# Kernel tuning notes

Hardware: AMD Instinct MI355X
Metric: run time of the kernel (lower is better)

## Reference

```python
import jax, jax.numpy as jnp
import numpy as np
import math

B, S, D, H = 2, 2048, 1024, 16
HD = D // H  # head_dim = 64
ROPE_BASE = 100000
EPS = 1e-09


def _linear_init(key, in_f, out_f):
    std = min(1.0, math.sqrt(out_f / in_f)) / math.sqrt(in_f)
    return jax.random.normal(key, (in_f, out_f)) * std


def setup_inputs() -> dict:
    key = jax.random.key(0)
    ks = jax.random.split(key, 7)
    Q = jax.random.normal(ks[0], (B, S, D), dtype=jnp.float32)
    K = jax.random.normal(ks[1], (B, S, D), dtype=jnp.float32)
    V = jax.random.normal(ks[2], (B, S, D), dtype=jnp.float32)
    mask = jnp.tril(jnp.ones((S, S), dtype=bool))  # causal
    Wq = _linear_init(ks[3], D, D)
    Wk = _linear_init(ks[4], D, D)
    Wv = _linear_init(ks[5], D, D)
    Wo = _linear_init(ks[6], D, D)
    return {"Q": Q, "K": K, "V": V, "mask": mask,
            "Wq": Wq, "Wk": Wk, "Wv": Wv, "Wo": Wo}


def _rope_tables(seq_len, d):
    positions = jnp.arange(0, seq_len)
    freqs = ROPE_BASE ** (jnp.arange(0, d, 2) / d)
    gamma = positions[:, None] * (1.0 / freqs)[None, :]  # [t, d/2]
    return jnp.cos(gamma).astype(jnp.bfloat16), jnp.sin(gamma).astype(jnp.bfloat16)


def _apply_rope(x, cos, sin):
    # x: [..., t, d]; cos/sin: [t, d/2]
    d = x.shape[-1]
    x1, x2 = x[..., : d // 2], x[..., d // 2:]
    y1 = x1 * cos + x2 * sin
    y2 = -x1 * sin + x2 * cos
    return jnp.concatenate([y1, y2], axis=-1)


def _rms_norm(x):
    rms = jnp.sqrt(jnp.mean(jnp.square(x), axis=-1, keepdims=True) + EPS)
    return x / rms


def reference(Q, K, V, mask, Wq, Wk, Wv, Wo):
    cos, sin = _rope_tables(S, HD)
    q = jnp.dot(Q, Wq)
    k = jnp.dot(K, Wk)
    v = jnp.dot(V, Wv)
    # [B, S, D] -> [B, H, S, HD]
    split = lambda t: t.reshape(*t.shape[:-1], H, HD).swapaxes(-3, -2)
    q, k, v = split(q), split(k), split(v)
    q = _rms_norm(_apply_rope(q, cos, sin))
    k = _rms_norm(_apply_rope(k, cos, sin))
    logits = jnp.einsum('bhqd,bhkd->bhqk', q, k) / jnp.sqrt(jnp.float32(HD))
    logits = jnp.where(mask[None, None, :, :], logits, -1000000000.0)
    attn = jax.nn.softmax(logits, axis=-1)
    vals = jnp.einsum('bhqk,bhkd->bhqd', attn, v)
    # [B, H, S, HD] -> [B, S, D]
    vals = vals.swapaxes(-3, -2).reshape(B, S, D)
    return jnp.dot(vals, Wo)
```

## Files before the change

kernel.cpp:

```cpp
#include <hip/hip_runtime.h>
#include <hip/hip_bf16.h>
#include <stdint.h>

typedef __hip_bfloat16 bf16;
typedef __attribute__((ext_vector_type(8))) short short8;
typedef __attribute__((ext_vector_type(4))) float float4v;

static constexpr int nB = 2, nS = 2048, nD = 1024, nH = 16, nHD = 64;
static constexpr int nBS = nB * nS;

#define AS_GLOBAL __attribute__((address_space(1)))
#define AS_LDS    __attribute__((address_space(3)))

union Frag16B { short8 v; uint4 u4; uint2 u2[2]; };

__device__ __forceinline__ void gload_lds16(const void* g, void* l) {
  __builtin_amdgcn_global_load_lds((AS_GLOBAL uint32_t*)(g), (AS_LDS uint32_t*)(l), 16, 0, 0);
}

__device__ __forceinline__ float fast_exp2(float x) {
#if __has_builtin(__builtin_amdgcn_exp2f)
  return __builtin_amdgcn_exp2f(x);
#else
  float r; asm volatile("v_exp_f32 %0, %1" : "=v"(r) : "v"(x)); return r;
#endif
}

__device__ __forceinline__ void lds_barrier() {
  asm volatile("s_waitcnt lgkmcnt(0)\ns_barrier" ::: "memory");
}

__global__ __launch_bounds__(256) void prep_kernel(
    const float* __restrict__ Qin, const float* __restrict__ Kin, const float* __restrict__ Vin,
    const float* __restrict__ Wq, const float* __restrict__ Wk,
    const float* __restrict__ Wv, const float* __restrict__ Wo,
    bf16* __restrict__ Qbf, bf16* __restrict__ Kbf, bf16* __restrict__ Vbf,
    bf16* __restrict__ WqT, bf16* __restrict__ WkT, bf16* __restrict__ WvT, bf16* __restrict__ WoT,
    bf16* __restrict__ cos_t, bf16* __restrict__ sin_t) {
  __shared__ float tile[64][65];
  int bx = blockIdx.x, t = threadIdx.x;
  if (bx < 3072) {
    int tz = bx >> 10, blk = bx & 1023;
    const float* src = tz == 0 ? Qin : tz == 1 ? Kin : Vin;
    bf16* dst = tz == 0 ? Qbf : tz == 1 ? Kbf : Vbf;
#pragma unroll
    for (int i = 0; i < 4; ++i) {
      int idx = blk * 1024 + i * 256 + t;
      float4 v = ((const float4*)src)[idx];
      union { bf16 b[4]; uint2 u; } tmp;
      tmp.b[0] = __float2bfloat16(v.x);
      tmp.b[1] = __float2bfloat16(v.y);
      tmp.b[2] = __float2bfloat16(v.z);
      tmp.b[3] = __float2bfloat16(v.w);
      ((uint2*)dst)[idx] = tmp.u;
    }
  } else if (bx < 4096) {
    int idx = bx - 3072;
    int z = idx >> 8;
    const float* W = z == 0 ? Wq : z == 1 ? Wk : z == 2 ? Wv : Wo;
    bf16* T = z == 0 ? WqT : z == 1 ? WkT : z == 2 ? WvT : WoT;
    int tk = (idx & 15) * 64, tn = ((idx >> 4) & 15) * 64;
    int c = t & 63, r0 = t >> 6;
#pragma unroll
    for (int i = 0; i < 16; ++i) {
      int r = i * 4 + r0;
      tile[r][c] = W[(size_t)(tk + r) * nD + tn + c];
    }
    __syncthreads();
#pragma unroll
    for (int i = 0; i < 16; ++i) {
      int r = i * 4 + r0;
      T[(size_t)(tn + r) * nD + tk + c] = __float2bfloat16(tile[c][r]);
    }
  } else {
    int base = (bx - 4096) * 1024 + t * 4;
#pragma unroll
    for (int i = 0; i < 4; ++i) {
      int e = base + i;
      int s = e >> 5, j = e & 31;
      float inv_freq = powf(100000.0f, -(float)(2 * j) / 64.0f);
      float g = (float)s * inv_freq;
      cos_t[e] = __float2bfloat16(cosf(g));
      sin_t[e] = __float2bfloat16(sinf(g));
    }
  }
}

__global__ __launch_bounds__(256) void gemm_qkv_kernel(
    const bf16* __restrict__ A0, const bf16* __restrict__ A1, const bf16* __restrict__ A2,
    const bf16* __restrict__ Bt0, const bf16* __restrict__ Bt1, const bf16* __restrict__ Bt2,
    bf16* __restrict__ q_h, bf16* __restrict__ k_h, bf16* __restrict__ vt_h,
    const bf16* __restrict__ cos_t, const bf16* __restrict__ sin_t) {
  const int z = blockIdx.z;
  const bf16* A  = z == 0 ? A0 : (z == 1 ? A1 : A2);
  const bf16* Bt = z == 0 ? Bt0 : (z == 1 ? Bt1 : Bt2);

  __shared__ bf16 As[128 * 32];
  __shared__ bf16 Bs[128 * 32];

  const int t = threadIdx.x;
  const int lane = t & 63;
  const int wid = t >> 6;
  const int quad = lane >> 4;
  const int l16 = lane & 15;
  const int wm = wid >> 1;
  const int wn = wid & 1;
  const int m0 = blockIdx.y * 128;
  const int n0 = blockIdx.x * 128;
  const int K = nD;

  float4v acc[4][4] = {};

  for (int kt = 0; kt < K; kt += 32) {
    __syncthreads();
#pragma unroll
    for (int p = 0; p < 2; ++p) {
      int cch = p * 256 + wid * 64 + lane;
      int row = cch >> 2, cc = cch & 3;
      gload_lds16(A + (size_t)(m0 + row) * K + kt + cc * 8, As + (size_t)(p * 256 + wid * 64) * 8);
      gload_lds16(Bt + (size_t)(n0 + row) * K + kt + cc * 8, Bs + (size_t)(p * 256 + wid * 64) * 8);
    }
    __syncthreads();

    Frag16B a[4], b[4];
#pragma unroll
    for (int mi = 0; mi < 4; ++mi)
      a[mi].u4 = *(const uint4*)&As[(wm * 64 + mi * 16 + l16) * 32 + quad * 8];
#pragma unroll
    for (int ni = 0; ni < 4; ++ni)
      b[ni].u4 = *(const uint4*)&Bs[(wn * 64 + ni * 16 + l16) * 32 + quad * 8];
#pragma unroll
    for (int mi = 0; mi < 4; ++mi)
#pragma unroll
      for (int ni = 0; ni < 4; ++ni)
        acc[mi][ni] = __builtin_amdgcn_mfma_f32_16x16x32_bf16(a[mi].v, b[ni].v, acc[mi][ni], 0, 0, 0);
  }

  const int col0 = n0 + wn * 64;
  if (z <= 1) {
    bf16* dst = z ? k_h : q_h;
#pragma unroll
    for (int mi = 0; mi < 4; ++mi)
#pragma unroll
      for (int r = 0; r < 4; ++r) {
        int row = m0 + wm * 64 + mi * 16 + quad * 4 + r;
        int s = row & (nS - 1);
        float x0 = acc[mi][0][r], x1 = acc[mi][1][r], x2 = acc[mi][2][r], x3 = acc[mi][3][r];
        float y[4];
#pragma unroll
        for (int p = 0; p < 2; ++p) {
          int d = p * 16 + l16;
          float c = __bfloat162float(cos_t[s * 32 + d]);
          float sn = __bfloat162float(sin_t[s * 32 + d]);
          float xa = p ? x1 : x0, xb = p ? x3 : x2;
          y[p] = xa * c + xb * sn;
          y[p + 2] = xb * c - xa * sn;
        }
        float ss = y[0] * y[0] + y[1] * y[1] + y[2] * y[2] + y[3] * y[3];
#pragma unroll
        for (int m = 1; m <= 8; m <<= 1) ss += __shfl_xor(ss, m, 64);
        float inv = 1.0f / sqrtf(ss * (1.0f / 64.0f) + 1e-9f);
#pragma unroll
        for (int ni = 0; ni < 4; ++ni)
          dst[(size_t)row * nD + col0 + ni * 16 + l16] = __float2bfloat16(y[ni] * inv);
      }
  } else {
#pragma unroll
    for (int mi = 0; mi < 4; ++mi)
#pragma unroll
      for (int r = 0; r < 4; ++r) {
        int row = m0 + wm * 64 + mi * 16 + quad * 4 + r;
        int b = row >> 11, s = row & (nS - 1);
#pragma unroll
        for (int ni = 0; ni < 4; ++ni) {
          int col = col0 + ni * 16 + l16;
          int h = col >> 6, d = col & 63;
          vt_h[((size_t)((b * nH + h) * 64 + d)) * nS + s] = __float2bfloat16(acc[mi][ni][r]);
        }
      }
  }
}

__global__ __launch_bounds__(256) void gemm_out_kernel(
    const bf16* __restrict__ A, const bf16* __restrict__ Bt, float* __restrict__ C) {
  __shared__ bf16 As[128 * 32];
  __shared__ bf16 Bs[128 * 32];
  const int t = threadIdx.x;
  const int lane = t & 63;
  const int wid = t >> 6;
  const int quad = lane >> 4;
  const int l16 = lane & 15;
  const int wm = wid >> 1;
  const int wn = wid & 1;
  const int m0 = blockIdx.y * 128;
  const int n0 = blockIdx.x * 128;
  const int K = nD;

  float4v acc[4][4] = {};
  for (int kt = 0; kt < K; kt += 32) {
    __syncthreads();
#pragma unroll
    for (int p = 0; p < 2; ++p) {
      int cch = p * 256 + wid * 64 + lane;
      int row = cch >> 2, cc = cch & 3;
      gload_lds16(A + (size_t)(m0 + row) * K + kt + cc * 8, As + (size_t)(p * 256 + wid * 64) * 8);
      gload_lds16(Bt + (size_t)(n0 + row) * K + kt + cc * 8, Bs + (size_t)(p * 256 + wid * 64) * 8);
    }
    __syncthreads();
    Frag16B a[4], b[4];
#pragma unroll
    for (int mi = 0; mi < 4; ++mi)
      a[mi].u4 = *(const uint4*)&As[(wm * 64 + mi * 16 + l16) * 32 + quad * 8];
#pragma unroll
    for (int ni = 0; ni < 4; ++ni)
      b[ni].u4 = *(const uint4*)&Bs[(wn * 64 + ni * 16 + l16) * 32 + quad * 8];
#pragma unroll
    for (int mi = 0; mi < 4; ++mi)
#pragma unroll
      for (int ni = 0; ni < 4; ++ni)
        acc[mi][ni] = __builtin_amdgcn_mfma_f32_16x16x32_bf16(a[mi].v, b[ni].v, acc[mi][ni], 0, 0, 0);
  }
#pragma unroll
  for (int mi = 0; mi < 4; ++mi)
#pragma unroll
    for (int ni = 0; ni < 4; ++ni)
#pragma unroll
      for (int r = 0; r < 4; ++r) {
        int row = m0 + wm * 64 + mi * 16 + quad * 4 + r;
        int col = n0 + wn * 64 + ni * 16 + l16;
        C[(size_t)row * nD + col] = acc[mi][ni][r];
      }
}

static constexpr int KSTR = 68;
static constexpr float SC = 0.18033688011112042f;

__global__ __launch_bounds__(256) void attn_kernel(const bf16* __restrict__ q_h,
                                                   const bf16* __restrict__ k_h,
                                                   const bf16* __restrict__ vt_h,
                                                   bf16* __restrict__ vals) {
  __shared__ bf16 Kl[2][64 * KSTR];
  __shared__ bf16 Vl[2][64 * KSTR];
  __shared__ bf16 Pl[4 * 16 * KSTR];

  const int t = threadIdx.x;
  const int lane = t & 63, wid = t >> 6, quad = lane >> 4, l16 = lane & 15;
  const int bh = blockIdx.y;
  const int b = bh >> 4, h = bh & 15;
  const int pairIdx = blockIdx.x;

  const bf16* Kbase = k_h + ((size_t)b * nS) * nD + h * 64;
  const bf16* Vbase = vt_h + (size_t)bh * 64 * nS;
  bf16* Pw = Pl + wid * 16 * KSTR;

  const int row0 = t >> 3;
  const int c8 = (t & 7) * 8;

  for (int phase = 0; phase < 2; ++phase) {
    const int qt = phase == 0 ? (31 - pairIdx) : pairIdx;
    const int n = qt + 1;

    Frag16B qf[2];
    {
      int qrow = qt * 64 + wid * 16 + l16;
      const bf16* qp = q_h + ((size_t)(b * nS + qrow)) * nD + h * 64;
      qf[0].u4 = *(const uint4*)(qp + quad * 8);
      qf[1].u4 = *(const uint4*)(qp + 32 + quad * 8);
    }

    uint4 kreg[2], vreg[2];
#pragma unroll
    for (int i = 0; i < 2; ++i) {
      kreg[i] = *(const uint4*)(Kbase + (size_t)(row0 + i * 32) * nD + c8);
      vreg[i] = *(const uint4*)(Vbase + (size_t)(row0 + i * 32) * nS + c8);
    }

    lds_barrier();

    float4v o_acc[4] = {};
    float l_i[4] = {0.f, 0.f, 0.f, 0.f};

    for (int kt = 0; kt < n; ++kt) {
      bf16* Kb = Kl[kt & 1];
      bf16* Vb = Vl[kt & 1];
#pragma unroll
      for (int i = 0; i < 2; ++i) {
        uint2 lo, hi;
        lo.x = kreg[i].x; lo.y = kreg[i].y; hi.x = kreg[i].z; hi.y = kreg[i].w;
        *(uint2*)&Kb[(row0 + i * 32) * KSTR + c8] = lo;
        *(uint2*)&Kb[(row0 + i * 32) * KSTR + c8 + 4] = hi;
        lo.x = vreg[i].x; lo.y = vreg[i].y; hi.x = vreg[i].z; hi.y = vreg[i].w;
        *(uint2*)&Vb[(row0 + i * 32) * KSTR + c8] = lo;
        *(uint2*)&Vb[(row0 + i * 32) * KSTR + c8 + 4] = hi;
      }
      if (kt + 1 < n) {
#pragma unroll
        for (int i = 0; i < 2; ++i) {
          kreg[i] = *(const uint4*)(Kbase + (size_t)((kt + 1) * 64 + row0 + i * 32) * nD + c8);
          vreg[i] = *(const uint4*)(Vbase + (size_t)(row0 + i * 32) * nS + (kt + 1) * 64 + c8);
        }
      }
      lds_barrier();

      float4v s_acc[4] = {};
#pragma unroll
      for (int ni = 0; ni < 4; ++ni) {
        Frag16B b0, b1;
        const bf16* kp = &Kb[(ni * 16 + l16) * KSTR + quad * 8];
        b0.u2[0] = *(const uint2*)(kp);
        b0.u2[1] = *(const uint2*)(kp + 4);
        b1.u2[0] = *(const uint2*)(kp + 32);
        b1.u2[1] = *(const uint2*)(kp + 36);
        s_acc[ni] = __builtin_amdgcn_mfma_f32_16x16x32_bf16(qf[0].v, b0.v, s_acc[ni], 0, 0, 0);
        s_acc[ni] = __builtin_amdgcn_mfma_f32_16x16x32_bf16(qf[1].v, b1.v, s_acc[ni], 0, 0, 0);
      }

      const bool diag = (kt == qt);
      const int qr0 = qt * 64 + wid * 16 + quad * 4;
#pragma unroll
      for (int ni = 0; ni < 4; ++ni) {
        int key = kt * 64 + ni * 16 + l16;
#pragma unroll
        for (int r = 0; r < 4; ++r) {
          float x = s_acc[ni][r] * SC;
          if (diag && key > qr0 + r) x = -12000.0f;
          float p = fast_exp2(x);
          l_i[r] += p;
          Pw[(quad * 4 + r) * KSTR + ni * 16 + l16] = __float2bfloat16(p);
        }
      }
      asm volatile("s_waitcnt lgkmcnt(0)" ::: "memory");

      Frag16B pa[2];
      const bf16* pp = &Pw[l16 * KSTR];
      pa[0].u2[0] = *(const uint2*)(pp + quad * 8);
      pa[0].u2[1] = *(const uint2*)(pp + quad * 8 + 4);
      pa[1].u2[0] = *(const uint2*)(pp + 32 + quad * 8);
      pa[1].u2[1] = *(const uint2*)(pp + 32 + quad * 8 + 4);
#pragma unroll
      for (int ni = 0; ni < 4; ++ni) {
        Frag16B vb0, vb1;
        const bf16* vp = &Vb[(ni * 16 + l16) * KSTR + quad * 8];
        vb0.u2[0] = *(const uint2*)(vp);
        vb0.u2[1] = *(const uint2*)(vp + 4);
        vb1.u2[0] = *(const uint2*)(vp + 32);
        vb1.u2[1] = *(const uint2*)(vp + 36);
        o_acc[ni] = __builtin_amdgcn_mfma_f32_16x16x32_bf16(pa[0].v, vb0.v, o_acc[ni], 0, 0, 0);
        o_acc[ni] = __builtin_amdgcn_mfma_f32_16x16x32_bf16(pa[1].v, vb1.v, o_acc[ni], 0, 0, 0);
      }
    }

#pragma unroll
    for (int r = 0; r < 4; ++r) {
#pragma unroll
      for (int m = 1; m <= 8; m <<= 1) l_i[r] += __shfl_xor(l_i[r], m, 64);
    }
    int qr0 = qt * 64 + wid * 16 + quad * 4;
#pragma unroll
    for (int ni = 0; ni < 4; ++ni)
#pragma unroll
      for (int r = 0; r < 4; ++r) {
        float o = o_acc[ni][r] / l_i[r];
        vals[((size_t)(b * nS + qr0 + r)) * nD + h * 64 + ni * 16 + l16] = __float2bfloat16(o);
      }
  }
}

extern "C" void kernel_launch(void* const* d_in, const int* in_sizes, int n_in,
                              void* d_out, int out_size, void* d_ws, size_t ws_size,
                              hipStream_t stream) {
  const float* Qin = (const float*)d_in[0];
  const float* Kin = (const float*)d_in[1];
  const float* Vin = (const float*)d_in[2];
  const float* Wq = (const float*)d_in[4];
  const float* Wk = (const float*)d_in[5];
  const float* Wv = (const float*)d_in[6];
  const float* Wo = (const float*)d_in[7];
  float* out = (float*)d_out;

  char* ws = (char*)d_ws;
  const size_t MB = 1u << 20;
  bf16* Qbf = (bf16*)(ws + 0 * MB);
  bf16* Kbf = (bf16*)(ws + 8 * MB);
  bf16* Vbf = (bf16*)(ws + 16 * MB);
  bf16* WqT = (bf16*)(ws + 24 * MB);
  bf16* WkT = (bf16*)(ws + 26 * MB);
  bf16* WvT = (bf16*)(ws + 28 * MB);
  bf16* WoT = (bf16*)(ws + 30 * MB);
  bf16* cos_t = (bf16*)(ws + 32 * MB);
  bf16* sin_t = (bf16*)(ws + 33 * MB);
  bf16* q_h = (bf16*)(ws + 34 * MB);
  bf16* k_h = (bf16*)(ws + 42 * MB);
  bf16* vt_h = (bf16*)(ws + 50 * MB);
  bf16* vals = (bf16*)(ws + 58 * MB);

  prep_kernel<<<4160, 256, 0, stream>>>(Qin, Kin, Vin, Wq, Wk, Wv, Wo,
                                        Qbf, Kbf, Vbf, WqT, WkT, WvT, WoT, cos_t, sin_t);

  gemm_qkv_kernel<<<dim3(8, 32, 3), 256, 0, stream>>>(Qbf, Kbf, Vbf, WqT, WkT, WvT,
                                                      q_h, k_h, vt_h, cos_t, sin_t);

  attn_kernel<<<dim3(16, 32), 256, 0, stream>>>(q_h, k_h, vt_h, vals);

  gemm_out_kernel<<<dim3(8, 32), 256, 0, stream>>>(vals, WoT, out);
}
```

Measured before the change: 243.4 us.

## Rework GEMMs with swizzled 64-wide K tiles and register-resident attention

```diff
diff --git a/kernel.cpp b/kernel.cpp
--- a/kernel.cpp
+++ b/kernel.cpp
@@ -4,6 +4,7 @@
 
 typedef __hip_bfloat16 bf16;
 typedef __attribute__((ext_vector_type(8))) short short8;
+typedef __attribute__((ext_vector_type(4))) short short4v;
 typedef __attribute__((ext_vector_type(4))) float float4v;
 
 static constexpr int nB = 2, nS = 2048, nD = 1024, nH = 16, nHD = 64;
@@ -24,10 +25,6 @@
 #else
   float r; asm volatile("v_exp_f32 %0, %1" : "=v"(r) : "v"(x)); return r;
 #endif
-}
-
-__device__ __forceinline__ void lds_barrier() {
-  asm volatile("s_waitcnt lgkmcnt(0)\ns_barrier" ::: "memory");
 }
 
 __global__ __launch_bounds__(256) void prep_kernel(
@@ -95,8 +92,8 @@
   const bf16* A  = z == 0 ? A0 : (z == 1 ? A1 : A2);
   const bf16* Bt = z == 0 ? Bt0 : (z == 1 ? Bt1 : Bt2);
 
-  __shared__ bf16 As[128 * 32];
-  __shared__ bf16 Bs[128 * 32];
+  __shared__ bf16 As[128 * 64];
+  __shared__ bf16 Bs[128 * 64];
 
   const int t = threadIdx.x;
   const int lane = t & 63;
@@ -105,35 +102,45 @@
   const int l16 = lane & 15;
   const int wm = wid >> 1;
   const int wn = wid & 1;
-  const int m0 = blockIdx.y * 128;
-  const int n0 = blockIdx.x * 128;
+  const int m0 = blockIdx.x * 128;
+  const int n0 = blockIdx.y * 128;
   const int K = nD;
+  const int rloc = lane >> 3, cl = lane & 7;
+  const int cg = cl ^ rloc;
 
   float4v acc[4][4] = {};
 
-  for (int kt = 0; kt < K; kt += 32) {
+  for (int kt = 0; kt < K; kt += 64) {
     __syncthreads();
 #pragma unroll
-    for (int p = 0; p < 2; ++p) {
-      int cch = p * 256 + wid * 64 + lane;
-      int row = cch >> 2, cc = cch & 3;
-      gload_lds16(A + (size_t)(m0 + row) * K + kt + cc * 8, As + (size_t)(p * 256 + wid * 64) * 8);
-      gload_lds16(Bt + (size_t)(n0 + row) * K + kt + cc * 8, Bs + (size_t)(p * 256 + wid * 64) * 8);
+    for (int p = 0; p < 4; ++p) {
+      int rowbase = (p * 4 + wid) * 8;
+      gload_lds16(A + (size_t)(m0 + rowbase + rloc) * K + kt + cg * 8, As + (size_t)rowbase * 64);
+      gload_lds16(Bt + (size_t)(n0 + rowbase + rloc) * K + kt + cg * 8, Bs + (size_t)rowbase * 64);
     }
     __syncthreads();
 
-    Frag16B a[4], b[4];
-#pragma unroll
-    for (int mi = 0; mi < 4; ++mi)
-      a[mi].u4 = *(const uint4*)&As[(wm * 64 + mi * 16 + l16) * 32 + quad * 8];
-#pragma unroll
-    for (int ni = 0; ni < 4; ++ni)
-      b[ni].u4 = *(const uint4*)&Bs[(wn * 64 + ni * 16 + l16) * 32 + quad * 8];
-#pragma unroll
-    for (int mi = 0; mi < 4; ++mi)
-#pragma unroll
-      for (int ni = 0; ni < 4; ++ni)
-        acc[mi][ni] = __builtin_amdgcn_mfma_f32_16x16x32_bf16(a[mi].v, b[ni].v, acc[mi][ni], 0, 0, 0);
+#pragma unroll
+    for (int ks = 0; ks < 2; ++ks) {
+      Frag16B a[4], b[4];
+#pragma unroll
+      for (int mi = 0; mi < 4; ++mi) {
+        int row = wm * 64 + mi * 16 + l16;
+        int ch = (ks * 4 + quad) ^ (row & 7);
+        a[mi].u4 = *(const uint4*)&As[row * 64 + ch * 8];
+      }
+#pragma unroll
+      for (int ni = 0; ni < 4; ++ni) {
+        int row = wn * 64 + ni * 16 + l16;
+        int ch = (ks * 4 + quad) ^ (row & 7);
+        b[ni].u4 = *(const uint4*)&Bs[row * 64 + ch * 8];
+      }
+#pragma unroll
+      for (int mi = 0; mi < 4; ++mi)
+#pragma unroll
+        for (int ni = 0; ni < 4; ++ni)
+          acc[mi][ni] = __builtin_amdgcn_mfma_f32_16x16x32_bf16(a[mi].v, b[ni].v, acc[mi][ni], 0, 0, 0);
+    }
   }
 
   const int col0 = n0 + wn * 64;
@@ -183,8 +190,8 @@
 
 __global__ __launch_bounds__(256) void gemm_out_kernel(
     const bf16* __restrict__ A, const bf16* __restrict__ Bt, float* __restrict__ C) {
-  __shared__ bf16 As[128 * 32];
-  __shared__ bf16 Bs[128 * 32];
+  __shared__ bf16 As[64 * 64];
+  __shared__ bf16 Bs[128 * 64];
   const int t = threadIdx.x;
   const int lane = t & 63;
   const int wid = t >> 6;
@@ -192,57 +199,67 @@
   const int l16 = lane & 15;
   const int wm = wid >> 1;
   const int wn = wid & 1;
-  const int m0 = blockIdx.y * 128;
-  const int n0 = blockIdx.x * 128;
+  const int m0 = blockIdx.x * 64;
+  const int n0 = blockIdx.y * 128;
   const int K = nD;
-
-  float4v acc[4][4] = {};
-  for (int kt = 0; kt < K; kt += 32) {
+  const int rloc = lane >> 3, cl = lane & 7;
+  const int cg = cl ^ rloc;
+
+  float4v acc[2][4] = {};
+  for (int kt = 0; kt < K; kt += 64) {
     __syncthreads();
 #pragma unroll
     for (int p = 0; p < 2; ++p) {
-      int cch = p * 256 + wid * 64 + lane;
-      int row = cch >> 2, cc = cch & 3;
-      gload_lds16(A + (size_t)(m0 + row) * K + kt + cc * 8, As + (size_t)(p * 256 + wid * 64) * 8);
-      gload_lds16(Bt + (size_t)(n0 + row) * K + kt + cc * 8, Bs + (size_t)(p * 256 + wid * 64) * 8);
+      int rowbase = (p * 4 + wid) * 8;
+      gload_lds16(A + (size_t)(m0 + rowbase + rloc) * K + kt + cg * 8, As + (size_t)rowbase * 64);
+    }
+#pragma unroll
+    for (int p = 0; p < 4; ++p) {
+      int rowbase = (p * 4 + wid) * 8;
+      gload_lds16(Bt + (size_t)(n0 + rowbase + rloc) * K + kt + cg * 8, Bs + (size_t)rowbase * 64);
     }
     __syncthreads();
-    Frag16B a[4], b[4];
-#pragma unroll
-    for (int mi = 0; mi < 4; ++mi)
-      a[mi].u4 = *(const uint4*)&As[(wm * 64 + mi * 16 + l16) * 32 + quad * 8];
+
+#pragma unroll
+    for (int ks = 0; ks < 2; ++ks) {
+      Frag16B a[2], b[4];
+#pragma unroll
+      for (int mi = 0; mi < 2; ++mi) {
+        int row = wm * 32 + mi * 16 + l16;
+        int ch = (ks * 4 + quad) ^ (row & 7);
+        a[mi].u4 = *(const uint4*)&As[row * 64 + ch * 8];
+      }
+#pragma unroll
+      for (int ni = 0; ni < 4; ++ni) {
+        int row = wn * 64 + ni * 16 + l16;
+        int ch = (ks * 4 + quad) ^ (row & 7);
+        b[ni].u4 = *(const uint4*)&Bs[row * 64 + ch * 8];
+      }
+#pragma unroll
+      for (int mi = 0; mi < 2; ++mi)
+#pragma unroll
+        for (int ni = 0; ni < 4; ++ni)
+          acc[mi][ni] = __builtin_amdgcn_mfma_f32_16x16x32_bf16(a[mi].v, b[ni].v, acc[mi][ni], 0, 0, 0);
+    }
+  }
+#pragma unroll
+  for (int mi = 0; mi < 2; ++mi)
 #pragma unroll
     for (int ni = 0; ni < 4; ++ni)
-      b[ni].u4 = *(const uint4*)&Bs[(wn * 64 + ni * 16 + l16) * 32 + quad * 8];
-#pragma unroll
-    for (int mi = 0; mi < 4; ++mi)
-#pragma unroll
-      for (int ni = 0; ni < 4; ++ni)
-        acc[mi][ni] = __builtin_amdgcn_mfma_f32_16x16x32_bf16(a[mi].v, b[ni].v, acc[mi][ni], 0, 0, 0);
-  }
-#pragma unroll
-  for (int mi = 0; mi < 4; ++mi)
-#pragma unroll
-    for (int ni = 0; ni < 4; ++ni)
 #pragma unroll
       for (int r = 0; r < 4; ++r) {
-        int row = m0 + wm * 64 + mi * 16 + quad * 4 + r;
+        int row = m0 + wm * 32 + mi * 16 + quad * 4 + r;
         int col = n0 + wn * 64 + ni * 16 + l16;
         C[(size_t)row * nD + col] = acc[mi][ni][r];
       }
 }
 
-static constexpr int KSTR = 68;
 static constexpr float SC = 0.18033688011112042f;
 
 __global__ __launch_bounds__(256) void attn_kernel(const bf16* __restrict__ q_h,
                                                    const bf16* __restrict__ k_h,
                                                    const bf16* __restrict__ vt_h,
                                                    bf16* __restrict__ vals) {
-  __shared__ bf16 Kl[2][64 * KSTR];
-  __shared__ bf16 Vl[2][64 * KSTR];
-  __shared__ bf16 Pl[4 * 16 * KSTR];
-
   const int t = threadIdx.x;
   const int lane = t & 63, wid = t >> 6, quad = lane >> 4, l16 = lane & 15;
   const int bh = blockIdx.y;
@@ -251,118 +268,95 @@
 
   const bf16* Kbase = k_h + ((size_t)b * nS) * nD + h * 64;
   const bf16* Vbase = vt_h + (size_t)bh * 64 * nS;
-  bf16* Pw = Pl + wid * 16 * KSTR;
-
-  const int row0 = t >> 3;
-  const int c8 = (t & 7) * 8;
 
   for (int phase = 0; phase < 2; ++phase) {
     const int qt = phase == 0 ? (31 - pairIdx) : pairIdx;
-    const int n = qt + 1;
+    const int q_global = qt * 64 + wid * 16 + l16;
 
     Frag16B qf[2];
     {
-      int qrow = qt * 64 + wid * 16 + l16;
-      const bf16* qp = q_h + ((size_t)(b * nS + qrow)) * nD + h * 64;
+      const bf16* qp = q_h + ((size_t)(b * nS + q_global)) * nD + h * 64;
       qf[0].u4 = *(const uint4*)(qp + quad * 8);
       qf[1].u4 = *(const uint4*)(qp + 32 + quad * 8);
     }
 
-    uint4 kreg[2], vreg[2];
-#pragma unroll
-    for (int i = 0; i < 2; ++i) {
-      kreg[i] = *(const uint4*)(Kbase + (size_t)(row0 + i * 32) * nD + c8);
-      vreg[i] = *(const uint4*)(Vbase + (size_t)(row0 + i * 32) * nS + c8);
-    }
-
-    lds_barrier();
-
     float4v o_acc[4] = {};
-    float l_i[4] = {0.f, 0.f, 0.f, 0.f};
-
-    for (int kt = 0; kt < n; ++kt) {
-      bf16* Kb = Kl[kt & 1];
-      bf16* Vb = Vl[kt & 1];
-#pragma unroll
-      for (int i = 0; i < 2; ++i) {
-        uint2 lo, hi;
-        lo.x = kreg[i].x; lo.y = kreg[i].y; hi.x = kreg[i].z; hi.y = kreg[i].w;
-        *(uint2*)&Kb[(row0 + i * 32) * KSTR + c8] = lo;
-        *(uint2*)&Kb[(row0 + i * 32) * KSTR + c8 + 4] = hi;
-        lo.x = vreg[i].x; lo.y = vreg[i].y; hi.x = vreg[i].z; hi.y = vreg[i].w;
-        *(uint2*)&Vb[(row0 + i * 32) * KSTR + c8] = lo;
-        *(uint2*)&Vb[(row0 + i * 32) * KSTR + c8 + 4] = hi;
-      }
-      if (kt + 1 < n) {
-#pragma unroll
-        for (int i = 0; i < 2; ++i) {
-          kreg[i] = *(const uint4*)(Kbase + (size_t)((kt + 1) * 64 + row0 + i * 32) * nD + c8);
-          vreg[i] = *(const uint4*)(Vbase + (size_t)(row0 + i * 32) * nS + (kt + 1) * 64 + c8);
+    float l_acc = 0.f;
+
+    Frag16B kf[4][2];
+#pragma unroll
+    for (int kt4 = 0; kt4 < 4; ++kt4) {
+      const bf16* kp = Kbase + (size_t)(kt4 * 16 + l16) * nD + quad * 8;
+      kf[kt4][0].u4 = *(const uint4*)(kp);
+      kf[kt4][1].u4 = *(const uint4*)(kp + 32);
+    }
+
+    for (int kt = 0; kt <= qt; ++kt) {
+      uint2 vf[4][4];
+#pragma unroll
+      for (int dt = 0; dt < 4; ++dt) {
+        const bf16* vp = Vbase + (size_t)(dt * 16 + l16) * nS + kt * 64 + quad * 4;
+#pragma unroll
+        for (int kt4 = 0; kt4 < 4; ++kt4)
+          vf[dt][kt4] = *(const uint2*)(vp + kt4 * 16);
+      }
+
+      float4v st[4];
+#pragma unroll
+      for (int kt4 = 0; kt4 < 4; ++kt4) {
+        float4v zz = {};
+        zz = __builtin_amdgcn_mfma_f32_16x16x32_bf16(kf[kt4][0].v, qf[0].v, zz, 0, 0, 0);
+        st[kt4] = __builtin_amdgcn_mfma_f32_16x16x32_bf16(kf[kt4][1].v, qf[1].v, zz, 0, 0, 0);
+      }
+
+      if (kt < qt) {
+#pragma unroll
+        for (int kt4 = 0; kt4 < 4; ++kt4) {
+          const bf16* kp = Kbase + (size_t)((kt + 1) * 64 + kt4 * 16 + l16) * nD + quad * 8;
+          kf[kt4][0].u4 = *(const uint4*)(kp);
+          kf[kt4][1].u4 = *(const uint4*)(kp + 32);
         }
       }
-      lds_barrier();
-
-      float4v s_acc[4] = {};
-#pragma unroll
-      for (int ni = 0; ni < 4; ++ni) {
-        Frag16B b0, b1;
-        const bf16* kp = &Kb[(ni * 16 + l16) * KSTR + quad * 8];
-        b0.u2[0] = *(const uint2*)(kp);
-        b0.u2[1] = *(const uint2*)(kp + 4);
-        b1.u2[0] = *(const uint2*)(kp + 32);
-        b1.u2[1] = *(const uint2*)(kp + 36);
-        s_acc[ni] = __builtin_amdgcn_mfma_f32_16x16x32_bf16(qf[0].v, b0.v, s_acc[ni], 0, 0, 0);
-        s_acc[ni] = __builtin_amdgcn_mfma_f32_16x16x32_bf16(qf[1].v, b1.v, s_acc[ni], 0, 0, 0);
-      }
-
+
+      short4v pf[4];
       const bool diag = (kt == qt);
-      const int qr0 = qt * 64 + wid * 16 + quad * 4;
-#pragma unroll
-      for (int ni = 0; ni < 4; ++ni) {
-        int key = kt * 64 + ni * 16 + l16;
+#pragma unroll
+      for (int kt4 = 0; kt4 < 4; ++kt4) {
+        int key0 = kt * 64 + kt4 * 16 + quad * 4;
 #pragma unroll
         for (int r = 0; r < 4; ++r) {
-          float x = s_acc[ni][r] * SC;
-          if (diag && key > qr0 + r) x = -12000.0f;
+          float x = st[kt4][r] * SC;
+          if (diag && (key0 + r) > q_global) x = -12000.0f;
           float p = fast_exp2(x);
-          l_i[r] += p;
-          Pw[(quad * 4 + r) * KSTR + ni * 16 + l16] = __float2bfloat16(p);
+          l_acc += p;
+          union { bf16 hh; short ss; } cv;
+          cv.hh = __float2bfloat16(p);
+          pf[kt4][r] = cv.ss;
         }
       }
-      asm volatile("s_waitcnt lgkmcnt(0)" ::: "memory");
-
-      Frag16B pa[2];
-      const bf16* pp = &Pw[l16 * KSTR];
-      pa[0].u2[0] = *(const uint2*)(pp + quad * 8);
-      pa[0].u2[1] = *(const uint2*)(pp + quad * 8 + 4);
-      pa[1].u2[0] = *(const uint2*)(pp + 32 + quad * 8);
-      pa[1].u2[1] = *(const uint2*)(pp + 32 + quad * 8 + 4);
-#pragma unroll
-      for (int ni = 0; ni < 4; ++ni) {
-        Frag16B vb0, vb1;
-        const bf16* vp = &Vb[(ni * 16 + l16) * KSTR + quad * 8];
-        vb0.u2[0] = *(const uint2*)(vp);
-        vb0.u2[1] = *(const uint2*)(vp + 4);
-        vb1.u2[0] = *(const uint2*)(vp + 32);
-        vb1.u2[1] = *(const uint2*)(vp + 36);
-        o_acc[ni] = __builtin_amdgcn_mfma_f32_16x16x32_bf16(pa[0].v, vb0.v, o_acc[ni], 0, 0, 0);
-        o_acc[ni] = __builtin_amdgcn_mfma_f32_16x16x32_bf16(pa[1].v, vb1.v, o_acc[ni], 0, 0, 0);
-      }
-    }
-
-#pragma unroll
-    for (int r = 0; r < 4; ++r) {
-#pragma unroll
-      for (int m = 1; m <= 8; m <<= 1) l_i[r] += __shfl_xor(l_i[r], m, 64);
-    }
-    int qr0 = qt * 64 + wid * 16 + quad * 4;
-#pragma unroll
-    for (int ni = 0; ni < 4; ++ni)
-#pragma unroll
-      for (int r = 0; r < 4; ++r) {
-        float o = o_acc[ni][r] / l_i[r];
-        vals[((size_t)(b * nS + qr0 + r)) * nD + h * 64 + ni * 16 + l16] = __float2bfloat16(o);
-      }
+
+#pragma unroll
+      for (int dt = 0; dt < 4; ++dt) {
+#pragma unroll
+        for (int kt4 = 0; kt4 < 4; ++kt4) {
+          union { uint2 u; short4v s; } vv;
+          vv.u = vf[dt][kt4];
+          o_acc[dt] = __builtin_amdgcn_mfma_f32_16x16x16bf16_1k(vv.s, pf[kt4], o_acc[dt], 0, 0, 0);
+        }
+      }
+    }
+
+    l_acc += __shfl_xor(l_acc, 16, 64);
+    l_acc += __shfl_xor(l_acc, 32, 64);
+    float inv_l = 1.0f / l_acc;
+
+#pragma unroll
+    for (int dt = 0; dt < 4; ++dt) {
+      union { bf16 b4[4]; uint2 u; } ov;
+#pragma unroll
+      for (int r = 0; r < 4; ++r) ov.b4[r] = __float2bfloat16(o_acc[dt][r] * inv_l);
+      *(uint2*)&vals[((size_t)(b * nS + q_global)) * nD + h * 64 + dt * 16 + quad * 4] = ov.u;
+    }
   }
 }
 
@@ -397,10 +391,10 @@
   prep_kernel<<<4160, 256, 0, stream>>>(Qin, Kin, Vin, Wq, Wk, Wv, Wo,
                                         Qbf, Kbf, Vbf, WqT, WkT, WvT, WoT, cos_t, sin_t);
 
-  gemm_qkv_kernel<<<dim3(8, 32, 3), 256, 0, stream>>>(Qbf, Kbf, Vbf, WqT, WkT, WvT,
+  gemm_qkv_kernel<<<dim3(32, 8, 3), 256, 0, stream>>>(Qbf, Kbf, Vbf, WqT, WkT, WvT,
                                                       q_h, k_h, vt_h, cos_t, sin_t);
 
   attn_kernel<<<dim3(16, 32), 256, 0, stream>>>(q_h, k_h, vt_h, vals);
 
-  gemm_out_kernel<<<dim3(8, 32), 256, 0, stream>>>(vals, WoT, out);
-}
+  gemm_out_kernel<<<dim3(64, 8), 256, 0, stream>>>(vals, WoT, out);
+}
```

Measured after the change: 355.2 us. +45.9%, slower.
